# Kernel tuning notes

Measured on AMD Instinct MI355X. Metric: run time of the kernel, lower is better.

Reference implementation:

```python
import jax, jax.numpy as jnp
import numpy as np

B, T, P, C = 32, 16, 16, 2048
EPS = 1e-5


def setup_inputs() -> dict:
    key = jax.random.key(0)
    ks = jax.random.split(key, 9)
    s = 0.02
    return {
        "X": jax.random.normal(ks[0], (B, T, P, C), dtype=jnp.float32),
        "W_att": jax.random.normal(ks[1], (C, C), dtype=jnp.float32) * s,
        "b_att": jnp.zeros((C,), dtype=jnp.float32),
        "W1": jax.random.normal(ks[2], (C, C), dtype=jnp.float32) * s,
        "b1": jnp.zeros((C,), dtype=jnp.float32),
        "gamma": jnp.ones((C,), dtype=jnp.float32),
        "beta": jnp.zeros((C,), dtype=jnp.float32),
        "W2": jax.random.normal(ks[3], (C, C), dtype=jnp.float32) * s,
        "b2": jnp.zeros((C,), dtype=jnp.float32),
    }


def reference(X, W_att, b_att, W1, b1, gamma, beta, W2, b2):
    b, t, p, c = X.shape
    Xf = X.reshape(b * t, p, c)                                   # [BT, P, C]
    # per-frame attention gate: mean over parts -> Linear -> sigmoid
    attn = jax.nn.sigmoid(jnp.einsum("nc,dc->nd", Xf.mean(axis=1), W_att) + b_att)
    Xg = Xf * attn[:, None, :]                                    # gate each part
    # gcn: Linear -> per-frame BatchNorm1d (training stats over P) -> ReLU -> Linear
    h = jnp.einsum("npc,dc->npd", Xg, W1) + b1                    # [BT, P, C]
    mu = h.mean(axis=1, keepdims=True)
    var = jnp.mean(jnp.square(h - mu), axis=1, keepdims=True)     # biased var, as torch BN
    hn = (h - mu) * jax.lax.rsqrt(var + EPS) * gamma + beta
    out = jnp.einsum("npc,dc->npd", jax.nn.relu(hn), W2) + b2
    return out.reshape(b, t, p, c)
```

## Files before the change

kernel.cpp:

```cpp
#include <hip/hip_runtime.h>
#include <hip/hip_bf16.h>

typedef __attribute__((ext_vector_type(8))) short short8;
typedef __attribute__((ext_vector_type(4))) float f32x4;

static constexpr int Cdim = 2048;
static constexpr int NFRM = 512;
static constexpr int Pdim = 16;
static constexpr int MROWS = NFRM * Pdim;
static constexpr float EPS = 1e-5f;

__device__ __forceinline__ unsigned short f2b(float x) {
  union { float f; unsigned u; } v; v.f = x;
  unsigned r = v.u + 0x7fffu + ((v.u >> 16) & 1u);
  return (unsigned short)(r >> 16);
}

__device__ __forceinline__ void gload16(const void* g, void* l) {
  __builtin_amdgcn_global_load_lds(
      (const __attribute__((address_space(1))) unsigned int*)g,
      (__attribute__((address_space(3))) unsigned int*)l, 16, 0, 0);
}


__global__ __launch_bounds__(256) void cast3_kernel(
    const float* __restrict__ s0, const float* __restrict__ s1, const float* __restrict__ s2,
    unsigned short* __restrict__ d0, unsigned short* __restrict__ d1, unsigned short* __restrict__ d2)
{
  long i = (long)blockIdx.x * 256 + threadIdx.x;
  const float* s; unsigned short* d; long off;
  if (i < 1048576)      { s = s0; d = d0; off = i; }
  else if (i < 2097152) { s = s1; d = d1; off = i - 1048576; }
  else                  { s = s2; d = d2; off = i - 2097152; }
  float4 v = reinterpret_cast<const float4*>(s)[off];
  union { unsigned short u[4]; unsigned long long q; } o;
  o.u[0] = f2b(v.x); o.u[1] = f2b(v.y); o.u[2] = f2b(v.z); o.u[3] = f2b(v.w);
  *reinterpret_cast<unsigned long long*>(d + off * 4) = o.q;
}

__global__ __launch_bounds__(256) void mean_cast_kernel(
    const float* __restrict__ X, unsigned short* __restrict__ Mb)
{
  int idx = blockIdx.x * 256 + threadIdx.x;
  int n  = idx >> 9;
  int c4 = idx & 511;
  const float4* xp = reinterpret_cast<const float4*>(X) + (long)n * (Pdim * 512) + c4;
  float4 s = {0.f, 0.f, 0.f, 0.f};
  #pragma unroll
  for (int p = 0; p < Pdim; ++p) {
    float4 v = xp[(long)p * 512];
    s.x += v.x; s.y += v.y; s.z += v.z; s.w += v.w;
  }
  const float r = 1.f / 16.f;
  union { unsigned short u[4]; unsigned long long q; } o;
  o.u[0] = f2b(s.x * r); o.u[1] = f2b(s.y * r); o.u[2] = f2b(s.z * r); o.u[3] = f2b(s.w * r);
  *reinterpret_cast<unsigned long long*>(Mb + (long)idx * 4) = o.q;
}

__global__ __launch_bounds__(256) void gate_kernel(
    const float* __restrict__ X, const float* __restrict__ P0, const float* __restrict__ P1,
    const float* __restrict__ b_att, unsigned short* __restrict__ Xg)
{
  long idx = (long)blockIdx.x * 256 + threadIdx.x;
  int c4 = (int)(idx & 511);
  long np = idx >> 9;
  long n  = np >> 4;
  float4 x  = reinterpret_cast<const float4*>(X)[idx];
  float4 p0 = reinterpret_cast<const float4*>(P0)[n * 512 + c4];
  float4 p1 = reinterpret_cast<const float4*>(P1)[n * 512 + c4];
  float4 bb = reinterpret_cast<const float4*>(b_att)[c4];
  float4 a;
  a.x = 1.f / (1.f + __expf(-(p0.x + p1.x + bb.x)));
  a.y = 1.f / (1.f + __expf(-(p0.y + p1.y + bb.y)));
  a.z = 1.f / (1.f + __expf(-(p0.z + p1.z + bb.z)));
  a.w = 1.f / (1.f + __expf(-(p0.w + p1.w + bb.w)));
  union { unsigned short u[4]; unsigned long long q; } o;
  o.u[0] = f2b(x.x * a.x); o.u[1] = f2b(x.y * a.y);
  o.u[2] = f2b(x.z * a.z); o.u[3] = f2b(x.w * a.w);
  *reinterpret_cast<unsigned long long*>(Xg + idx * 4) = o.q;
}

__global__ __launch_bounds__(256) void gemm_att_sk(
    const unsigned short* __restrict__ A,
    const unsigned short* __restrict__ B,
    float* __restrict__ P)
{
  constexpr int N = 2048, K = 2048, KH = 1024;
  __shared__ unsigned short As[128 * 32];
  __shared__ unsigned short Bs[128 * 32];
  const int t = threadIdx.x;
  const int lane = t & 63;
  const int wid = t >> 6;
  const int wr = wid >> 1, wc = wid & 1;
  const int m0 = blockIdx.x * 128, n0 = blockIdx.y * 128;
  const int k0 = blockIdx.z * KH;
  float* out = P + (long)blockIdx.z * (512L * 2048);

  f32x4 acc[4][4];
  #pragma unroll
  for (int i = 0; i < 4; i++)
    #pragma unroll
    for (int j = 0; j < 4; j++) acc[i][j] = (f32x4){0.f, 0.f, 0.f, 0.f};

  const int srow = t >> 2;
  const int scol = (t & 3) * 8;
  const long aoff0 = (long)(m0 + srow) * K + scol;
  const long aoff1 = (long)(m0 + 64 + srow) * K + scol;
  const long boff0 = (long)(n0 + srow) * K + scol;
  const long boff1 = (long)(n0 + 64 + srow) * K + scol;
  char* AsB = (char*)As;
  char* BsB = (char*)Bs;

  const int fr = lane & 15;
  const int fk = (lane >> 4) * 8;

  for (int kt = k0; kt < k0 + KH; kt += 32) {
    __syncthreads();
    gload16(A + aoff0 + kt, AsB + t * 16);
    gload16(A + aoff1 + kt, AsB + 4096 + t * 16);
    gload16(B + boff0 + kt, BsB + t * 16);
    gload16(B + boff1 + kt, BsB + 4096 + t * 16);
    __syncthreads();
    short8 af[4], bfr[4];
    #pragma unroll
    for (int m = 0; m < 4; m++)
      af[m] = *reinterpret_cast<const short8*>(&As[(wr * 64 + m * 16 + fr) * 32 + fk]);
    #pragma unroll
    for (int n = 0; n < 4; n++)
      bfr[n] = *reinterpret_cast<const short8*>(&Bs[(wc * 64 + n * 16 + fr) * 32 + fk]);
    #pragma unroll
    for (int m = 0; m < 4; m++)
      #pragma unroll
      for (int n = 0; n < 4; n++)
        acc[m][n] = __builtin_amdgcn_mfma_f32_16x16x32_bf16(af[m], bfr[n], acc[m][n], 0, 0, 0);
  }

  const int l4 = lane >> 4;
  #pragma unroll
  for (int m = 0; m < 4; m++) {
    const int r0 = m0 + wr * 64 + m * 16 + l4 * 4;
    #pragma unroll
    for (int n = 0; n < 4; n++) {
      const int cn = n0 + wc * 64 + n * 16 + fr;
      #pragma unroll
      for (int j = 0; j < 4; j++)
        out[(long)(r0 + j) * N + cn] = acc[m][n][j];
    }
  }
}

template<int EPI>
__global__ __launch_bounds__(512, 2) void gemm256(
    const unsigned short* __restrict__ A,
    const unsigned short* __restrict__ Bp,
    int Kk, int Nn, int nbx,
    const float* __restrict__ bias,
    const float* __restrict__ gamma,
    const float* __restrict__ beta,
    float* __restrict__ Cf,
    unsigned short* __restrict__ Cb)
{
  __shared__ char lds[131072];
  const int t = threadIdx.x;
  const int lane = t & 63;
  const int wid = t >> 6;
  const int wr = wid >> 2;
  const int wc = wid & 3;

  const int nw = gridDim.x;
  const int wg = (blockIdx.x & 7) * (nw >> 3) + (blockIdx.x >> 3);
  const int bx = wg % nbx;
  const int by = wg / nbx;
  const int m0 = bx << 8, n0 = by << 8;

  const int NT = Kk >> 6;
  const int NI = NT >> 1;

  const long h64 = (long)64 * Kk, h128 = (long)128 * Kk;
  const int row0 = t >> 3;
  const int col0 = ((t & 7) * 8) ^ ((row0 & 7) << 3);
  const unsigned short* gA = A  + (long)(m0 + row0) * Kk + col0;
  const unsigned short* gB = Bp + (long)(n0 + row0) * Kk + col0;

  const int fr_ = lane & 15;
  const int cb0 = ((lane >> 4) << 4) ^ ((fr_ & 7) << 4);
  const int aB = (wr << 14) + fr_ * 128;
  const int bB = 32768 + ((wc >> 1) << 14) + ((wc & 1) << 13) + fr_ * 128;

#define STG(gp_, ko_, lo_) do { \
    const unsigned short* g0_ = (gp_) + (ko_); \
    gload16(g0_, lds + (lo_) + (t << 4)); \
    gload16(g0_ + h64, lds + (lo_) + 8192 + (t << 4)); } while (0)

#define LDSA(buf_, m_, ks_) (*(const short8*)(lds + (buf_) * 65536 + aB + (m_) * 2048 + (cb0 ^ ((ks_) << 6))))
#define LDSB(buf_, n_, ks_) (*(const short8*)(lds + (buf_) * 65536 + bB + (n_) * 2048 + (cb0 ^ ((ks_) << 6))))

#define RDAF(buf_, mb_) do { \
    af[0][0] = LDSA(buf_, (mb_) + 0, 0); af[0][1] = LDSA(buf_, (mb_) + 0, 1); \
    af[1][0] = LDSA(buf_, (mb_) + 1, 0); af[1][1] = LDSA(buf_, (mb_) + 1, 1); \
    af[2][0] = LDSA(buf_, (mb_) + 2, 0); af[2][1] = LDSA(buf_, (mb_) + 2, 1); \
    af[3][0] = LDSA(buf_, (mb_) + 3, 0); af[3][1] = LDSA(buf_, (mb_) + 3, 1); } while (0)

#define RDB(buf_, nb_, dst_) do { \
    dst_[0][0] = LDSB(buf_, (nb_) + 0, 0); dst_[0][1] = LDSB(buf_, (nb_) + 0, 1); \
    dst_[1][0] = LDSB(buf_, (nb_) + 1, 0); dst_[1][1] = LDSB(buf_, (nb_) + 1, 1); } while (0)

#define QUAD(mb_, nb_, b_) do { \
    _Pragma("unroll") \
    for (int mi = 0; mi < 4; ++mi) { \
      _Pragma("unroll") \
      for (int ni = 0; ni < 2; ++ni) { \
        acc[(mb_) + mi][(nb_) + ni] = __builtin_amdgcn_mfma_f32_16x16x32_bf16(af[mi][0], b_[ni][0], acc[(mb_) + mi][(nb_) + ni], 0, 0, 0); \
        acc[(mb_) + mi][(nb_) + ni] = __builtin_amdgcn_mfma_f32_16x16x32_bf16(af[mi][1], b_[ni][1], acc[(mb_) + mi][(nb_) + ni], 0, 0, 0); \
      } } } while (0)

#define BARX() do { \
    __builtin_amdgcn_sched_barrier(0); \
    __builtin_amdgcn_s_barrier(); \
    asm volatile("s_waitcnt lgkmcnt(0)" ::: "memory"); \
    __builtin_amdgcn_sched_barrier(0); } while (0)

#define PRIO1() __builtin_amdgcn_s_setprio(1)
#define PRIO0() __builtin_amdgcn_s_setprio(0)
#define VMC(n_) asm volatile("s_waitcnt vmcnt(" #n_ ")" ::: "memory")

  f32x4 acc[8][4];
  #pragma unroll
  for (int i = 0; i < 8; i++)
    #pragma unroll
    for (int j = 0; j < 4; j++) acc[i][j] = (f32x4){0.f, 0.f, 0.f, 0.f};

  short8 af[4][2], b23[2][2], b0E[2][2], b0O[2][2];

  STG(gA, 0, 0);
  STG(gA + h128, 0, 16384);
  STG(gB, 0, 32768);
  STG(gB + h128, 0, 49152);
  STG(gB, 64, 98304);
  STG(gB + h128, 64, 114688);
  VMC(4);
  __builtin_amdgcn_s_barrier();
  __builtin_amdgcn_sched_barrier(0);
  RDB(0, 0, b0E);

#define ITERBODY(LAST_) do { \
     \
    STG(gA, ko + 64, 65536); \
    RDAF(0, 0); \
    BARX(); PRIO1(); QUAD(0, 0, b0E); PRIO0(); \
     \
    STG(gA + h128, ko + 64, 81920); \
    RDB(0, 2, b23); \
    BARX(); PRIO1(); QUAD(0, 2, b23); PRIO0(); \
     \
    VMC(4); \
    if (!(LAST_)) STG(gB, ko + 128, 32768); \
    RDAF(0, 4); \
    BARX(); PRIO1(); QUAD(4, 0, b0E); PRIO0(); \
     \
    if (LAST_) { VMC(0); } else { VMC(2); STG(gB + h128, ko + 128, 49152); } \
    RDB(1, 0, b0O); \
    BARX(); PRIO1(); QUAD(4, 2, b23); PRIO0(); \
     \
    if (!(LAST_)) STG(gA, ko + 128, 0); \
    RDAF(1, 0); \
    BARX(); PRIO1(); QUAD(0, 0, b0O); PRIO0(); \
     \
    if (!(LAST_)) STG(gA + h128, ko + 128, 16384); \
    RDB(1, 2, b23); \
    BARX(); PRIO1(); QUAD(0, 2, b23); PRIO0(); \
     \
    if (!(LAST_)) { VMC(4); STG(gB, ko + 192, 98304); } \
    RDAF(1, 4); \
    BARX(); PRIO1(); QUAD(4, 0, b0O); PRIO0(); \
     \
    if (!(LAST_)) { VMC(2); STG(gB + h128, ko + 192, 114688); RDB(0, 0, b0E); } \
    BARX(); PRIO1(); QUAD(4, 2, b23); PRIO0(); \
  } while (0)

  long ko = 0;
  for (int i = 0; i < NI - 1; ++i, ko += 128) {
    ITERBODY(0);
  }
  ITERBODY(1);

  const int l4 = lane >> 4;
  #pragma unroll
  for (int m = 0; m < 8; ++m) {
    const int r0 = m0 + wr * 128 + m * 16 + l4 * 4;
    #pragma unroll
    for (int n = 0; n < 4; ++n) {
      const int cn = n0 + wc * 64 + n * 16 + fr_;
      if constexpr (EPI == 1) {
        float s1 = 0.f, s2 = 0.f;
        #pragma unroll
        for (int j = 0; j < 4; j++) { float v = acc[m][n][j]; s1 += v; s2 += v * v; }
        s1 += __shfl_xor(s1, 16); s2 += __shfl_xor(s2, 16);
        s1 += __shfl_xor(s1, 32); s2 += __shfl_xor(s2, 32);
        const float mean = s1 * 0.0625f;
        const float var  = s2 * 0.0625f - mean * mean;
        const float sc = rsqrtf(var + EPS) * gamma[cn];
        const float sh = beta[cn] - mean * sc;
        #pragma unroll
        for (int j = 0; j < 4; j++) {
          float v = fmaxf(acc[m][n][j] * sc + sh, 0.f);
          Cb[(long)(r0 + j) * Nn + cn] = f2b(v);
        }
      } else {
        const float bb = bias[cn];
        #pragma unroll
        for (int j = 0; j < 4; j++)
          Cf[(long)(r0 + j) * Nn + cn] = acc[m][n][j] + bb;
      }
    }
  }
#undef STG
#undef LDSA
#undef LDSB
#undef RDAF
#undef RDB
#undef QUAD
#undef BARX
#undef PRIO1
#undef PRIO0
#undef VMC
#undef ITERBODY
}

extern "C" void kernel_launch(void* const* d_in, const int* in_sizes, int n_in,
                              void* d_out, int out_size, void* d_ws, size_t ws_size,
                              hipStream_t stream) {
  const float* X     = (const float*)d_in[0];
  const float* W_att = (const float*)d_in[1];
  const float* b_att = (const float*)d_in[2];
  const float* W1    = (const float*)d_in[3];
  const float* gamma = (const float*)d_in[5];
  const float* beta  = (const float*)d_in[6];
  const float* W2    = (const float*)d_in[7];
  const float* b2    = (const float*)d_in[8];
  float* out = (float*)d_out;

  char* ws = (char*)d_ws;
  unsigned short* Wab = (unsigned short*)(ws + 0);
  unsigned short* W1b = (unsigned short*)(ws + 8388608);
  unsigned short* W2b = (unsigned short*)(ws + 16777216);
  float*          Pat = (float*)        (ws + 25165824);
  unsigned short* Xg  = (unsigned short*)(ws + 33554432);
  unsigned short* Hr  = (unsigned short*)(ws + 67108864);
  unsigned short* Mb  = (unsigned short*)(ws + 67108864);

  hipLaunchKernelGGL(cast3_kernel, dim3(12288), dim3(256), 0, stream,
                     W_att, W1, W2, Wab, W1b, W2b);
  hipLaunchKernelGGL(mean_cast_kernel, dim3(1024), dim3(256), 0, stream, X, Mb);
  hipLaunchKernelGGL(gemm_att_sk, dim3(4, 16, 2), dim3(256), 0, stream,
                     Mb, Wab, Pat);
  hipLaunchKernelGGL(gate_kernel, dim3(16384), dim3(256), 0, stream,
                     X, Pat, Pat + 512L * 2048, b_att, Xg);
  hipLaunchKernelGGL((gemm256<1>), dim3(256), dim3(512), 0, stream,
                     Xg, W1b, Cdim, Cdim, 32, nullptr, gamma, beta, nullptr, Hr);
  hipLaunchKernelGGL((gemm256<2>), dim3(256), dim3(512), 0, stream,
                     Hr, W2b, Cdim, Cdim, 32, b2, nullptr, nullptr, out, nullptr);
}
```

Measured before the change: 188.4 us.

## Use 32x32x16 MFMA in main GEMMs and split attention GEMM four ways

The two large 256x256 GEMMs now use the 32x32x16 bf16 MFMA instead of 16x16x32, with new LDS fragment addressing and an epilogue adjusted to the 32x32 accumulator layout, including BatchNorm statistics over 16-row groups. Larger MFMA tiles mean fewer instructions and fewer LDS fragment reads per FLOP. Separately, the attention GEMM split-K goes from 2 to 4 slices to put more blocks on the device, and the gate kernel sums four partials. The extra partial buffer is placed in workspace that aliases the Mb/Hr region, so correctness depends on those buffers not being live at the same time.

```diff
diff --git a/kernel.cpp b/kernel.cpp
--- a/kernel.cpp
+++ b/kernel.cpp
@@ -3,6 +3,7 @@
 
 typedef __attribute__((ext_vector_type(8))) short short8;
 typedef __attribute__((ext_vector_type(4))) float f32x4;
+typedef __attribute__((ext_vector_type(16))) float f32x16;
 
 static constexpr int Cdim = 2048;
 static constexpr int NFRM = 512;
@@ -58,22 +59,25 @@
 }
 
 __global__ __launch_bounds__(256) void gate_kernel(
-    const float* __restrict__ X, const float* __restrict__ P0, const float* __restrict__ P1,
+    const float* __restrict__ X, const float* __restrict__ PA, const float* __restrict__ PB,
     const float* __restrict__ b_att, unsigned short* __restrict__ Xg)
 {
+  constexpr long F = 512L * 2048;
   long idx = (long)blockIdx.x * 256 + threadIdx.x;
   int c4 = (int)(idx & 511);
   long np = idx >> 9;
   long n  = np >> 4;
   float4 x  = reinterpret_cast<const float4*>(X)[idx];
-  float4 p0 = reinterpret_cast<const float4*>(P0)[n * 512 + c4];
-  float4 p1 = reinterpret_cast<const float4*>(P1)[n * 512 + c4];
+  float4 p0 = reinterpret_cast<const float4*>(PA)[n * 512 + c4];
+  float4 p1 = reinterpret_cast<const float4*>(PA + F)[n * 512 + c4];
+  float4 p2 = reinterpret_cast<const float4*>(PB)[n * 512 + c4];
+  float4 p3 = reinterpret_cast<const float4*>(PB + F)[n * 512 + c4];
   float4 bb = reinterpret_cast<const float4*>(b_att)[c4];
   float4 a;
-  a.x = 1.f / (1.f + __expf(-(p0.x + p1.x + bb.x)));
-  a.y = 1.f / (1.f + __expf(-(p0.y + p1.y + bb.y)));
-  a.z = 1.f / (1.f + __expf(-(p0.z + p1.z + bb.z)));
-  a.w = 1.f / (1.f + __expf(-(p0.w + p1.w + bb.w)));
+  a.x = 1.f / (1.f + __expf(-(p0.x + p1.x + p2.x + p3.x + bb.x)));
+  a.y = 1.f / (1.f + __expf(-(p0.y + p1.y + p2.y + p3.y + bb.y)));
+  a.z = 1.f / (1.f + __expf(-(p0.z + p1.z + p2.z + p3.z + bb.z)));
+  a.w = 1.f / (1.f + __expf(-(p0.w + p1.w + p2.w + p3.w + bb.w)));
   union { unsigned short u[4]; unsigned long long q; } o;
   o.u[0] = f2b(x.x * a.x); o.u[1] = f2b(x.y * a.y);
   o.u[2] = f2b(x.z * a.z); o.u[3] = f2b(x.w * a.w);
@@ -83,9 +87,10 @@
 __global__ __launch_bounds__(256) void gemm_att_sk(
     const unsigned short* __restrict__ A,
     const unsigned short* __restrict__ B,
-    float* __restrict__ P)
-{
-  constexpr int N = 2048, K = 2048, KH = 1024;
+    float* __restrict__ PA, float* __restrict__ PB)
+{
+  constexpr int N = 2048, K = 2048, KH = 512;
+  constexpr long F = 512L * 2048;
   __shared__ unsigned short As[128 * 32];
   __shared__ unsigned short Bs[128 * 32];
   const int t = threadIdx.x;
@@ -94,7 +99,7 @@
   const int wr = wid >> 1, wc = wid & 1;
   const int m0 = blockIdx.x * 128, n0 = blockIdx.y * 128;
   const int k0 = blockIdx.z * KH;
-  float* out = P + (long)blockIdx.z * (512L * 2048);
+  float* out = (blockIdx.z < 2) ? (PA + (long)blockIdx.z * F) : (PB + (long)(blockIdx.z - 2) * F);
 
   f32x4 acc[4][4];
   #pragma unroll
@@ -182,36 +187,35 @@
   const unsigned short* gA = A  + (long)(m0 + row0) * Kk + col0;
   const unsigned short* gB = Bp + (long)(n0 + row0) * Kk + col0;
 
-  const int fr_ = lane & 15;
-  const int cb0 = ((lane >> 4) << 4) ^ ((fr_ & 7) << 4);
-  const int aB = (wr << 14) + fr_ * 128;
-  const int bB = 32768 + ((wc >> 1) << 14) + ((wc & 1) << 13) + fr_ * 128;
+  const int fr32 = lane & 31;
+  const int cb32 = (((lane >> 5) << 4)) ^ ((lane & 7) << 4);
+  const int aB32 = (wr << 14) + fr32 * 128;
+  const int bB32 = 32768 + ((wc >> 1) << 14) + (((wc & 1) << 6) + fr32) * 128;
 
 #define STG(gp_, ko_, lo_) do { \
     const unsigned short* g0_ = (gp_) + (ko_); \
     gload16(g0_, lds + (lo_) + (t << 4)); \
     gload16(g0_ + h64, lds + (lo_) + 8192 + (t << 4)); } while (0)
 
-#define LDSA(buf_, m_, ks_) (*(const short8*)(lds + (buf_) * 65536 + aB + (m_) * 2048 + (cb0 ^ ((ks_) << 6))))
-#define LDSB(buf_, n_, ks_) (*(const short8*)(lds + (buf_) * 65536 + bB + (n_) * 2048 + (cb0 ^ ((ks_) << 6))))
-
-#define RDAF(buf_, mb_) do { \
-    af[0][0] = LDSA(buf_, (mb_) + 0, 0); af[0][1] = LDSA(buf_, (mb_) + 0, 1); \
-    af[1][0] = LDSA(buf_, (mb_) + 1, 0); af[1][1] = LDSA(buf_, (mb_) + 1, 1); \
-    af[2][0] = LDSA(buf_, (mb_) + 2, 0); af[2][1] = LDSA(buf_, (mb_) + 2, 1); \
-    af[3][0] = LDSA(buf_, (mb_) + 3, 0); af[3][1] = LDSA(buf_, (mb_) + 3, 1); } while (0)
-
-#define RDB(buf_, nb_, dst_) do { \
-    dst_[0][0] = LDSB(buf_, (nb_) + 0, 0); dst_[0][1] = LDSB(buf_, (nb_) + 0, 1); \
-    dst_[1][0] = LDSB(buf_, (nb_) + 1, 0); dst_[1][1] = LDSB(buf_, (nb_) + 1, 1); } while (0)
-
-#define QUAD(mb_, nb_, b_) do { \
+#define LDSA32(buf_, mh_, ml_, ks_) (*(const short8*)(lds + (buf_) * 65536 + aB32 + (mh_) * 8192 + (ml_) * 4096 + (cb32 ^ ((ks_) << 5))))
+#define LDSB32(buf_, nh_, ks_)      (*(const short8*)(lds + (buf_) * 65536 + bB32 + (nh_) * 4096 + (cb32 ^ ((ks_) << 5))))
+
+#define RDA32(buf_, mh_) do { \
+    af[0][0] = LDSA32(buf_, mh_, 0, 0); af[0][1] = LDSA32(buf_, mh_, 0, 1); \
+    af[0][2] = LDSA32(buf_, mh_, 0, 2); af[0][3] = LDSA32(buf_, mh_, 0, 3); \
+    af[1][0] = LDSA32(buf_, mh_, 1, 0); af[1][1] = LDSA32(buf_, mh_, 1, 1); \
+    af[1][2] = LDSA32(buf_, mh_, 1, 2); af[1][3] = LDSA32(buf_, mh_, 1, 3); } while (0)
+
+#define RDB32(buf_, nh_, dst_) do { \
+    dst_[0] = LDSB32(buf_, nh_, 0); dst_[1] = LDSB32(buf_, nh_, 1); \
+    dst_[2] = LDSB32(buf_, nh_, 2); dst_[3] = LDSB32(buf_, nh_, 3); } while (0)
+
+#define QUAD32(mh_, nh_, b_) do { \
     _Pragma("unroll") \
-    for (int mi = 0; mi < 4; ++mi) { \
+    for (int ml = 0; ml < 2; ++ml) { \
       _Pragma("unroll") \
-      for (int ni = 0; ni < 2; ++ni) { \
-        acc[(mb_) + mi][(nb_) + ni] = __builtin_amdgcn_mfma_f32_16x16x32_bf16(af[mi][0], b_[ni][0], acc[(mb_) + mi][(nb_) + ni], 0, 0, 0); \
-        acc[(mb_) + mi][(nb_) + ni] = __builtin_amdgcn_mfma_f32_16x16x32_bf16(af[mi][1], b_[ni][1], acc[(mb_) + mi][(nb_) + ni], 0, 0, 0); \
+      for (int ks = 0; ks < 4; ++ks) { \
+        acc[(mh_) * 2 + ml][nh_] = __builtin_amdgcn_mfma_f32_32x32x16_bf16(af[ml][ks], b_[ks], acc[(mh_) * 2 + ml][nh_], 0, 0, 0); \
       } } } while (0)
 
 #define BARX() do { \
@@ -224,13 +228,15 @@
 #define PRIO0() __builtin_amdgcn_s_setprio(0)
 #define VMC(n_) asm volatile("s_waitcnt vmcnt(" #n_ ")" ::: "memory")
 
-  f32x4 acc[8][4];
-  #pragma unroll
-  for (int i = 0; i < 8; i++)
-    #pragma unroll
-    for (int j = 0; j < 4; j++) acc[i][j] = (f32x4){0.f, 0.f, 0.f, 0.f};
-
-  short8 af[4][2], b23[2][2], b0E[2][2], b0O[2][2];
+  f32x16 acc[4][2];
+  #pragma unroll
+  for (int i = 0; i < 4; i++)
+    #pragma unroll
+    for (int j = 0; j < 2; j++)
+      #pragma unroll
+      for (int e = 0; e < 16; e++) acc[i][j][e] = 0.f;
+
+  short8 af[2][4], b1s[4], bE0[4], bO0[4];
 
   STG(gA, 0, 0);
   STG(gA + h128, 0, 16384);
@@ -241,41 +247,41 @@
   VMC(4);
   __builtin_amdgcn_s_barrier();
   __builtin_amdgcn_sched_barrier(0);
-  RDB(0, 0, b0E);
+  RDB32(0, 0, bE0);
 
 #define ITERBODY(LAST_) do { \
      \
     STG(gA, ko + 64, 65536); \
-    RDAF(0, 0); \
-    BARX(); PRIO1(); QUAD(0, 0, b0E); PRIO0(); \
+    RDA32(0, 0); \
+    BARX(); PRIO1(); QUAD32(0, 0, bE0); PRIO0(); \
      \
     STG(gA + h128, ko + 64, 81920); \
-    RDB(0, 2, b23); \
-    BARX(); PRIO1(); QUAD(0, 2, b23); PRIO0(); \
+    RDB32(0, 1, b1s); \
+    BARX(); PRIO1(); QUAD32(0, 1, b1s); PRIO0(); \
      \
     VMC(4); \
     if (!(LAST_)) STG(gB, ko + 128, 32768); \
-    RDAF(0, 4); \
-    BARX(); PRIO1(); QUAD(4, 0, b0E); PRIO0(); \
+    RDA32(0, 1); \
+    BARX(); PRIO1(); QUAD32(1, 0, bE0); PRIO0(); \
      \
     if (LAST_) { VMC(0); } else { VMC(2); STG(gB + h128, ko + 128, 49152); } \
-    RDB(1, 0, b0O); \
-    BARX(); PRIO1(); QUAD(4, 2, b23); PRIO0(); \
+    RDB32(1, 0, bO0); \
+    BARX(); PRIO1(); QUAD32(1, 1, b1s); PRIO0(); \
      \
     if (!(LAST_)) STG(gA, ko + 128, 0); \
-    RDAF(1, 0); \
-    BARX(); PRIO1(); QUAD(0, 0, b0O); PRIO0(); \
+    RDA32(1, 0); \
+    BARX(); PRIO1(); QUAD32(0, 0, bO0); PRIO0(); \
      \
     if (!(LAST_)) STG(gA + h128, ko + 128, 16384); \
-    RDB(1, 2, b23); \
-    BARX(); PRIO1(); QUAD(0, 2, b23); PRIO0(); \
+    RDB32(1, 1, b1s); \
+    BARX(); PRIO1(); QUAD32(0, 1, b1s); PRIO0(); \
      \
     if (!(LAST_)) { VMC(4); STG(gB, ko + 192, 98304); } \
-    RDAF(1, 4); \
-    BARX(); PRIO1(); QUAD(4, 0, b0O); PRIO0(); \
-     \
-    if (!(LAST_)) { VMC(2); STG(gB + h128, ko + 192, 114688); RDB(0, 0, b0E); } \
-    BARX(); PRIO1(); QUAD(4, 2, b23); PRIO0(); \
+    RDA32(1, 1); \
+    BARX(); PRIO1(); QUAD32(1, 0, bO0); PRIO0(); \
+     \
+    if (!(LAST_)) { VMC(2); STG(gB + h128, ko + 192, 114688); RDB32(0, 0, bE0); } \
+    BARX(); PRIO1(); QUAD32(1, 1, b1s); PRIO0(); \
   } while (0)
 
   long ko = 0;
@@ -284,42 +290,48 @@
   }
   ITERBODY(1);
 
-  const int l4 = lane >> 4;
-  #pragma unroll
-  for (int m = 0; m < 8; ++m) {
-    const int r0 = m0 + wr * 128 + m * 16 + l4 * 4;
-    #pragma unroll
-    for (int n = 0; n < 4; ++n) {
-      const int cn = n0 + wc * 64 + n * 16 + fr_;
+  const int hi = lane >> 5;
+  #pragma unroll
+  for (int mt = 0; mt < 4; ++mt) {
+    const int rbase = m0 + wr * 128 + mt * 32;
+    #pragma unroll
+    for (int nh = 0; nh < 2; ++nh) {
+      const int cn = n0 + wc * 64 + nh * 32 + fr32;
       if constexpr (EPI == 1) {
-        float s1 = 0.f, s2 = 0.f;
+        const float g_ = gamma[cn], b_ = beta[cn];
         #pragma unroll
-        for (int j = 0; j < 4; j++) { float v = acc[m][n][j]; s1 += v; s2 += v * v; }
-        s1 += __shfl_xor(s1, 16); s2 += __shfl_xor(s2, 16);
-        s1 += __shfl_xor(s1, 32); s2 += __shfl_xor(s2, 32);
-        const float mean = s1 * 0.0625f;
-        const float var  = s2 * 0.0625f - mean * mean;
-        const float sc = rsqrtf(var + EPS) * gamma[cn];
-        const float sh = beta[cn] - mean * sc;
-        #pragma unroll
-        for (int j = 0; j < 4; j++) {
-          float v = fmaxf(acc[m][n][j] * sc + sh, 0.f);
-          Cb[(long)(r0 + j) * Nn + cn] = f2b(v);
+        for (int f = 0; f < 2; ++f) {
+          float s1 = 0.f, s2 = 0.f;
+          #pragma unroll
+          for (int j = 0; j < 8; ++j) { float v = acc[mt][nh][f * 8 + j]; s1 += v; s2 += v * v; }
+          s1 += __shfl_xor(s1, 32); s2 += __shfl_xor(s2, 32);
+          const float mean = s1 * 0.0625f;
+          const float var  = s2 * 0.0625f - mean * mean;
+          const float sc = rsqrtf(var + EPS) * g_;
+          const float sh = b_ - mean * sc;
+          #pragma unroll
+          for (int j = 0; j < 8; ++j) {
+            const int row = rbase + f * 16 + (j & 3) + 8 * (j >> 2) + 4 * hi;
+            float v = fmaxf(acc[mt][nh][f * 8 + j] * sc + sh, 0.f);
+            Cb[(long)row * Nn + cn] = f2b(v);
+          }
         }
       } else {
         const float bb = bias[cn];
         #pragma unroll
-        for (int j = 0; j < 4; j++)
-          Cf[(long)(r0 + j) * Nn + cn] = acc[m][n][j] + bb;
+        for (int r = 0; r < 16; ++r) {
+          const int row = rbase + (r & 3) + 8 * (r >> 2) + 4 * hi;
+          Cf[(long)row * Nn + cn] = acc[mt][nh][r] + bb;
+        }
       }
     }
   }
 #undef STG
-#undef LDSA
-#undef LDSB
-#undef RDAF
-#undef RDB
-#undef QUAD
+#undef LDSA32
+#undef LDSB32
+#undef RDA32
+#undef RDB32
+#undef QUAD32
 #undef BARX
 #undef PRIO1
 #undef PRIO0
@@ -344,18 +356,19 @@
   unsigned short* Wab = (unsigned short*)(ws + 0);
   unsigned short* W1b = (unsigned short*)(ws + 8388608);
   unsigned short* W2b = (unsigned short*)(ws + 16777216);
-  float*          Pat = (float*)        (ws + 25165824);
+  float*          PatA= (float*)        (ws + 25165824);
   unsigned short* Xg  = (unsigned short*)(ws + 33554432);
   unsigned short* Hr  = (unsigned short*)(ws + 67108864);
   unsigned short* Mb  = (unsigned short*)(ws + 67108864);
+  float*          PatB= (float*)        (ws + 67108864 + 2097152);
 
   hipLaunchKernelGGL(cast3_kernel, dim3(12288), dim3(256), 0, stream,
                      W_att, W1, W2, Wab, W1b, W2b);
   hipLaunchKernelGGL(mean_cast_kernel, dim3(1024), dim3(256), 0, stream, X, Mb);
-  hipLaunchKernelGGL(gemm_att_sk, dim3(4, 16, 2), dim3(256), 0, stream,
-                     Mb, Wab, Pat);
+  hipLaunchKernelGGL(gemm_att_sk, dim3(4, 16, 4), dim3(256), 0, stream,
+                     Mb, Wab, PatA, PatB);
   hipLaunchKernelGGL(gate_kernel, dim3(16384), dim3(256), 0, stream,
-                     X, Pat, Pat + 512L * 2048, b_att, Xg);
+                     X, PatA, PatB, b_att, Xg);
   hipLaunchKernelGGL((gemm256<1>), dim3(256), dim3(512), 0, stream,
                      Xg, W1b, Cdim, Cdim, 32, nullptr, gamma, beta, nullptr, Hr);
   hipLaunchKernelGGL((gemm256<2>), dim3(256), dim3(512), 0, stream,
```

Result: slower. 201.9 us (+7.1%).

## Raise attention GEMM split-K to four and double-buffer A fragments in main GEMM

Applied to the files above, without the earlier changes.

The attention-gate GEMM now splits K four ways instead of two, giving 256 blocks instead of 128 so more CUs have work; the gate kernel sums four partial buffers, with the extra two stored in a second workspace region. The main 256-tile GEMM pipeline is reworked so A fragments use two register sets and the next LDS reads are issued right after each barrier. Partial lgkmcnt waits replace the full wait, so LDS reads overlap the MFMA work. This costs more registers and extra partial-sum traffic, and depends on the waitcnt counts being exactly right.

```diff
diff --git a/kernel.cpp b/kernel.cpp
--- a/kernel.cpp
+++ b/kernel.cpp
@@ -58,22 +58,25 @@
 }
 
 __global__ __launch_bounds__(256) void gate_kernel(
-    const float* __restrict__ X, const float* __restrict__ P0, const float* __restrict__ P1,
+    const float* __restrict__ X, const float* __restrict__ PA, const float* __restrict__ PB,
     const float* __restrict__ b_att, unsigned short* __restrict__ Xg)
 {
+  constexpr long F = 512L * 2048;
   long idx = (long)blockIdx.x * 256 + threadIdx.x;
   int c4 = (int)(idx & 511);
   long np = idx >> 9;
   long n  = np >> 4;
   float4 x  = reinterpret_cast<const float4*>(X)[idx];
-  float4 p0 = reinterpret_cast<const float4*>(P0)[n * 512 + c4];
-  float4 p1 = reinterpret_cast<const float4*>(P1)[n * 512 + c4];
+  float4 p0 = reinterpret_cast<const float4*>(PA)[n * 512 + c4];
+  float4 p1 = reinterpret_cast<const float4*>(PA + F)[n * 512 + c4];
+  float4 p2 = reinterpret_cast<const float4*>(PB)[n * 512 + c4];
+  float4 p3 = reinterpret_cast<const float4*>(PB + F)[n * 512 + c4];
   float4 bb = reinterpret_cast<const float4*>(b_att)[c4];
   float4 a;
-  a.x = 1.f / (1.f + __expf(-(p0.x + p1.x + bb.x)));
-  a.y = 1.f / (1.f + __expf(-(p0.y + p1.y + bb.y)));
-  a.z = 1.f / (1.f + __expf(-(p0.z + p1.z + bb.z)));
-  a.w = 1.f / (1.f + __expf(-(p0.w + p1.w + bb.w)));
+  a.x = 1.f / (1.f + __expf(-(p0.x + p1.x + p2.x + p3.x + bb.x)));
+  a.y = 1.f / (1.f + __expf(-(p0.y + p1.y + p2.y + p3.y + bb.y)));
+  a.z = 1.f / (1.f + __expf(-(p0.z + p1.z + p2.z + p3.z + bb.z)));
+  a.w = 1.f / (1.f + __expf(-(p0.w + p1.w + p2.w + p3.w + bb.w)));
   union { unsigned short u[4]; unsigned long long q; } o;
   o.u[0] = f2b(x.x * a.x); o.u[1] = f2b(x.y * a.y);
   o.u[2] = f2b(x.z * a.z); o.u[3] = f2b(x.w * a.w);
@@ -83,9 +86,10 @@
 __global__ __launch_bounds__(256) void gemm_att_sk(
     const unsigned short* __restrict__ A,
     const unsigned short* __restrict__ B,
-    float* __restrict__ P)
-{
-  constexpr int N = 2048, K = 2048, KH = 1024;
+    float* __restrict__ PA, float* __restrict__ PB)
+{
+  constexpr int N = 2048, K = 2048, KH = 512;
+  constexpr long F = 512L * 2048;
   __shared__ unsigned short As[128 * 32];
   __shared__ unsigned short Bs[128 * 32];
   const int t = threadIdx.x;
@@ -94,7 +98,7 @@
   const int wr = wid >> 1, wc = wid & 1;
   const int m0 = blockIdx.x * 128, n0 = blockIdx.y * 128;
   const int k0 = blockIdx.z * KH;
-  float* out = P + (long)blockIdx.z * (512L * 2048);
+  float* out = (blockIdx.z < 2) ? (PA + (long)blockIdx.z * F) : (PB + (long)(blockIdx.z - 2) * F);
 
   f32x4 acc[4][4];
   #pragma unroll
@@ -195,29 +199,32 @@
 #define LDSA(buf_, m_, ks_) (*(const short8*)(lds + (buf_) * 65536 + aB + (m_) * 2048 + (cb0 ^ ((ks_) << 6))))
 #define LDSB(buf_, n_, ks_) (*(const short8*)(lds + (buf_) * 65536 + bB + (n_) * 2048 + (cb0 ^ ((ks_) << 6))))
 
-#define RDAF(buf_, mb_) do { \
-    af[0][0] = LDSA(buf_, (mb_) + 0, 0); af[0][1] = LDSA(buf_, (mb_) + 0, 1); \
-    af[1][0] = LDSA(buf_, (mb_) + 1, 0); af[1][1] = LDSA(buf_, (mb_) + 1, 1); \
-    af[2][0] = LDSA(buf_, (mb_) + 2, 0); af[2][1] = LDSA(buf_, (mb_) + 2, 1); \
-    af[3][0] = LDSA(buf_, (mb_) + 3, 0); af[3][1] = LDSA(buf_, (mb_) + 3, 1); } while (0)
+#define RDAF(buf_, mb_, dst_) do { \
+    dst_[0][0] = LDSA(buf_, (mb_) + 0, 0); dst_[0][1] = LDSA(buf_, (mb_) + 0, 1); \
+    dst_[1][0] = LDSA(buf_, (mb_) + 1, 0); dst_[1][1] = LDSA(buf_, (mb_) + 1, 1); \
+    dst_[2][0] = LDSA(buf_, (mb_) + 2, 0); dst_[2][1] = LDSA(buf_, (mb_) + 2, 1); \
+    dst_[3][0] = LDSA(buf_, (mb_) + 3, 0); dst_[3][1] = LDSA(buf_, (mb_) + 3, 1); } while (0)
 
 #define RDB(buf_, nb_, dst_) do { \
     dst_[0][0] = LDSB(buf_, (nb_) + 0, 0); dst_[0][1] = LDSB(buf_, (nb_) + 0, 1); \
     dst_[1][0] = LDSB(buf_, (nb_) + 1, 0); dst_[1][1] = LDSB(buf_, (nb_) + 1, 1); } while (0)
 
-#define QUAD(mb_, nb_, b_) do { \
+#define QUAD(mb_, nb_, a_, b_) do { \
     _Pragma("unroll") \
     for (int mi = 0; mi < 4; ++mi) { \
       _Pragma("unroll") \
       for (int ni = 0; ni < 2; ++ni) { \
-        acc[(mb_) + mi][(nb_) + ni] = __builtin_amdgcn_mfma_f32_16x16x32_bf16(af[mi][0], b_[ni][0], acc[(mb_) + mi][(nb_) + ni], 0, 0, 0); \
-        acc[(mb_) + mi][(nb_) + ni] = __builtin_amdgcn_mfma_f32_16x16x32_bf16(af[mi][1], b_[ni][1], acc[(mb_) + mi][(nb_) + ni], 0, 0, 0); \
+        acc[(mb_) + mi][(nb_) + ni] = __builtin_amdgcn_mfma_f32_16x16x32_bf16(a_[mi][0], b_[ni][0], acc[(mb_) + mi][(nb_) + ni], 0, 0, 0); \
+        acc[(mb_) + mi][(nb_) + ni] = __builtin_amdgcn_mfma_f32_16x16x32_bf16(a_[mi][1], b_[ni][1], acc[(mb_) + mi][(nb_) + ni], 0, 0, 0); \
       } } } while (0)
 
 #define BARX() do { \
     __builtin_amdgcn_sched_barrier(0); \
     __builtin_amdgcn_s_barrier(); \
-    asm volatile("s_waitcnt lgkmcnt(0)" ::: "memory"); \
+    __builtin_amdgcn_sched_barrier(0); } while (0)
+
+#define LGK(n_) do { \
+    asm volatile("s_waitcnt lgkmcnt(" #n_ ")" ::: "memory"); \
     __builtin_amdgcn_sched_barrier(0); } while (0)
 
 #define PRIO1() __builtin_amdgcn_s_setprio(1)
@@ -230,7 +237,7 @@
     #pragma unroll
     for (int j = 0; j < 4; j++) acc[i][j] = (f32x4){0.f, 0.f, 0.f, 0.f};
 
-  short8 af[4][2], b23[2][2], b0E[2][2], b0O[2][2];
+  short8 afA[4][2], afB[4][2], b23[2][2], bE0[2][2], bO0[2][2];
 
   STG(gA, 0, 0);
   STG(gA + h128, 0, 16384);
@@ -241,41 +248,51 @@
   VMC(4);
   __builtin_amdgcn_s_barrier();
   __builtin_amdgcn_sched_barrier(0);
-  RDB(0, 0, b0E);
+  RDAF(0, 0, afA);
+  RDB(0, 0, bE0);
+  __builtin_amdgcn_sched_barrier(0);
 
 #define ITERBODY(LAST_) do { \
      \
     STG(gA, ko + 64, 65536); \
-    RDAF(0, 0); \
-    BARX(); PRIO1(); QUAD(0, 0, b0E); PRIO0(); \
+    BARX(); \
+    RDB(0, 2, b23); \
+    LGK(4); PRIO1(); QUAD(0, 0, afA, bE0); PRIO0(); \
      \
     STG(gA + h128, ko + 64, 81920); \
-    RDB(0, 2, b23); \
-    BARX(); PRIO1(); QUAD(0, 2, b23); PRIO0(); \
-     \
-    VMC(4); \
-    if (!(LAST_)) STG(gB, ko + 128, 32768); \
-    RDAF(0, 4); \
-    BARX(); PRIO1(); QUAD(4, 0, b0E); PRIO0(); \
-     \
-    if (LAST_) { VMC(0); } else { VMC(2); STG(gB + h128, ko + 128, 49152); } \
-    RDB(1, 0, b0O); \
-    BARX(); PRIO1(); QUAD(4, 2, b23); PRIO0(); \
+    BARX(); \
+    RDAF(0, 4, afB); \
+    LGK(8); PRIO1(); QUAD(0, 2, afA, b23); PRIO0(); \
+     \
+    if (LAST_) { VMC(6); } else { VMC(8); STG(gB, ko + 128, 32768); } \
+    BARX(); \
+    RDB(1, 0, bO0); \
+    LGK(4); PRIO1(); QUAD(4, 0, afB, bE0); PRIO0(); \
+     \
+    if (LAST_) { VMC(0); } else { VMC(4); STG(gB + h128, ko + 128, 49152); } \
+    BARX(); \
+    RDAF(1, 0, afA); \
+    LGK(12); PRIO1(); QUAD(4, 2, afB, b23); PRIO0(); \
      \
     if (!(LAST_)) STG(gA, ko + 128, 0); \
-    RDAF(1, 0); \
-    BARX(); PRIO1(); QUAD(0, 0, b0O); PRIO0(); \
+    BARX(); \
+    RDB(1, 2, b23); \
+    LGK(4); PRIO1(); QUAD(0, 0, afA, bO0); PRIO0(); \
      \
     if (!(LAST_)) STG(gA + h128, ko + 128, 16384); \
-    RDB(1, 2, b23); \
-    BARX(); PRIO1(); QUAD(0, 2, b23); PRIO0(); \
-     \
-    if (!(LAST_)) { VMC(4); STG(gB, ko + 192, 98304); } \
-    RDAF(1, 4); \
-    BARX(); PRIO1(); QUAD(4, 0, b0O); PRIO0(); \
-     \
-    if (!(LAST_)) { VMC(2); STG(gB + h128, ko + 192, 114688); RDB(0, 0, b0E); } \
-    BARX(); PRIO1(); QUAD(4, 2, b23); PRIO0(); \
+    BARX(); \
+    RDAF(1, 4, afB); \
+    LGK(8); PRIO1(); QUAD(0, 2, afA, b23); PRIO0(); \
+     \
+    if (!(LAST_)) { VMC(8); STG(gB, ko + 192, 98304); } \
+    BARX(); \
+    if (!(LAST_)) { RDB(0, 0, bE0); LGK(4); } else { LGK(0); } \
+    PRIO1(); QUAD(4, 0, afB, bO0); PRIO0(); \
+     \
+    if (!(LAST_)) { VMC(4); STG(gB + h128, ko + 192, 114688); } \
+    BARX(); \
+    if (!(LAST_)) { RDAF(0, 0, afA); LGK(12); } else { LGK(0); } \
+    PRIO1(); QUAD(4, 2, afB, b23); PRIO0(); \
   } while (0)
 
   long ko = 0;
@@ -321,6 +338,7 @@
 #undef RDB
 #undef QUAD
 #undef BARX
+#undef LGK
 #undef PRIO1
 #undef PRIO0
 #undef VMC
@@ -344,18 +362,19 @@
   unsigned short* Wab = (unsigned short*)(ws + 0);
   unsigned short* W1b = (unsigned short*)(ws + 8388608);
   unsigned short* W2b = (unsigned short*)(ws + 16777216);
-  float*          Pat = (float*)        (ws + 25165824);
+  float*          PatA= (float*)        (ws + 25165824);
   unsigned short* Xg  = (unsigned short*)(ws + 33554432);
   unsigned short* Hr  = (unsigned short*)(ws + 67108864);
   unsigned short* Mb  = (unsigned short*)(ws + 67108864);
+  float*          PatB= (float*)        (ws + 67108864 + 2097152);
 
   hipLaunchKernelGGL(cast3_kernel, dim3(12288), dim3(256), 0, stream,
                      W_att, W1, W2, Wab, W1b, W2b);
   hipLaunchKernelGGL(mean_cast_kernel, dim3(1024), dim3(256), 0, stream, X, Mb);
-  hipLaunchKernelGGL(gemm_att_sk, dim3(4, 16, 2), dim3(256), 0, stream,
-                     Mb, Wab, Pat);
+  hipLaunchKernelGGL(gemm_att_sk, dim3(4, 16, 4), dim3(256), 0, stream,
+                     Mb, Wab, PatA, PatB);
   hipLaunchKernelGGL(gate_kernel, dim3(16384), dim3(256), 0, stream,
-                     X, Pat, Pat + 512L * 2048, b_att, Xg);
+                     X, PatA, PatB, b_att, Xg);
   hipLaunchKernelGGL((gemm256<1>), dim3(256), dim3(512), 0, stream,
                      Xg, W1b, Cdim, Cdim, 32, nullptr, gamma, beta, nullptr, Hr);
   hipLaunchKernelGGL((gemm256<2>), dim3(256), dim3(512), 0, stream,
```

Measured after the change: 469.6 us. 149% more time.

## Split attention GEMM four ways along K and drop LDS wait in barrier macro

Applied to the files above, without the earlier changes.

The attention-gate GEMM now splits K into four slices instead of two, launching twice as many blocks. This gives the 512x2048 problem more parallelism across the CUs. The gate kernel now sums four partial buffers, and the extra two partials live in a workspace region that is later reused for Hr. Separately, the explicit lgkmcnt(0) wait is removed from the barrier macro in the main GEMM pipeline to cut stalls. That relies on the compiler's own waits for LDS reads and risks races with the async global-to-LDS stores.

```diff
diff --git a/kernel.cpp b/kernel.cpp
--- a/kernel.cpp
+++ b/kernel.cpp
@@ -58,22 +58,25 @@
 }
 
 __global__ __launch_bounds__(256) void gate_kernel(
-    const float* __restrict__ X, const float* __restrict__ P0, const float* __restrict__ P1,
+    const float* __restrict__ X, const float* __restrict__ PA, const float* __restrict__ PB,
     const float* __restrict__ b_att, unsigned short* __restrict__ Xg)
 {
+  constexpr long F = 512L * 2048;
   long idx = (long)blockIdx.x * 256 + threadIdx.x;
   int c4 = (int)(idx & 511);
   long np = idx >> 9;
   long n  = np >> 4;
   float4 x  = reinterpret_cast<const float4*>(X)[idx];
-  float4 p0 = reinterpret_cast<const float4*>(P0)[n * 512 + c4];
-  float4 p1 = reinterpret_cast<const float4*>(P1)[n * 512 + c4];
+  float4 p0 = reinterpret_cast<const float4*>(PA)[n * 512 + c4];
+  float4 p1 = reinterpret_cast<const float4*>(PA + F)[n * 512 + c4];
+  float4 p2 = reinterpret_cast<const float4*>(PB)[n * 512 + c4];
+  float4 p3 = reinterpret_cast<const float4*>(PB + F)[n * 512 + c4];
   float4 bb = reinterpret_cast<const float4*>(b_att)[c4];
   float4 a;
-  a.x = 1.f / (1.f + __expf(-(p0.x + p1.x + bb.x)));
-  a.y = 1.f / (1.f + __expf(-(p0.y + p1.y + bb.y)));
-  a.z = 1.f / (1.f + __expf(-(p0.z + p1.z + bb.z)));
-  a.w = 1.f / (1.f + __expf(-(p0.w + p1.w + bb.w)));
+  a.x = 1.f / (1.f + __expf(-(p0.x + p1.x + p2.x + p3.x + bb.x)));
+  a.y = 1.f / (1.f + __expf(-(p0.y + p1.y + p2.y + p3.y + bb.y)));
+  a.z = 1.f / (1.f + __expf(-(p0.z + p1.z + p2.z + p3.z + bb.z)));
+  a.w = 1.f / (1.f + __expf(-(p0.w + p1.w + p2.w + p3.w + bb.w)));
   union { unsigned short u[4]; unsigned long long q; } o;
   o.u[0] = f2b(x.x * a.x); o.u[1] = f2b(x.y * a.y);
   o.u[2] = f2b(x.z * a.z); o.u[3] = f2b(x.w * a.w);
@@ -83,9 +86,10 @@
 __global__ __launch_bounds__(256) void gemm_att_sk(
     const unsigned short* __restrict__ A,
     const unsigned short* __restrict__ B,
-    float* __restrict__ P)
-{
-  constexpr int N = 2048, K = 2048, KH = 1024;
+    float* __restrict__ PA, float* __restrict__ PB)
+{
+  constexpr int N = 2048, K = 2048, KH = 512;
+  constexpr long F = 512L * 2048;
   __shared__ unsigned short As[128 * 32];
   __shared__ unsigned short Bs[128 * 32];
   const int t = threadIdx.x;
@@ -94,7 +98,7 @@
   const int wr = wid >> 1, wc = wid & 1;
   const int m0 = blockIdx.x * 128, n0 = blockIdx.y * 128;
   const int k0 = blockIdx.z * KH;
-  float* out = P + (long)blockIdx.z * (512L * 2048);
+  float* out = (blockIdx.z < 2) ? (PA + (long)blockIdx.z * F) : (PB + (long)(blockIdx.z - 2) * F);
 
   f32x4 acc[4][4];
   #pragma unroll
@@ -217,7 +221,6 @@
 #define BARX() do { \
     __builtin_amdgcn_sched_barrier(0); \
     __builtin_amdgcn_s_barrier(); \
-    asm volatile("s_waitcnt lgkmcnt(0)" ::: "memory"); \
     __builtin_amdgcn_sched_barrier(0); } while (0)
 
 #define PRIO1() __builtin_amdgcn_s_setprio(1)
@@ -230,7 +233,7 @@
     #pragma unroll
     for (int j = 0; j < 4; j++) acc[i][j] = (f32x4){0.f, 0.f, 0.f, 0.f};
 
-  short8 af[4][2], b23[2][2], b0E[2][2], b0O[2][2];
+  short8 af[4][2], b23[2][2], bE0[2][2], bO0[2][2];
 
   STG(gA, 0, 0);
   STG(gA + h128, 0, 16384);
@@ -241,13 +244,13 @@
   VMC(4);
   __builtin_amdgcn_s_barrier();
   __builtin_amdgcn_sched_barrier(0);
-  RDB(0, 0, b0E);
+  RDB(0, 0, bE0);
 
 #define ITERBODY(LAST_) do { \
      \
     STG(gA, ko + 64, 65536); \
     RDAF(0, 0); \
-    BARX(); PRIO1(); QUAD(0, 0, b0E); PRIO0(); \
+    BARX(); PRIO1(); QUAD(0, 0, bE0); PRIO0(); \
      \
     STG(gA + h128, ko + 64, 81920); \
     RDB(0, 2, b23); \
@@ -256,15 +259,15 @@
     VMC(4); \
     if (!(LAST_)) STG(gB, ko + 128, 32768); \
     RDAF(0, 4); \
-    BARX(); PRIO1(); QUAD(4, 0, b0E); PRIO0(); \
+    BARX(); PRIO1(); QUAD(4, 0, bE0); PRIO0(); \
      \
     if (LAST_) { VMC(0); } else { VMC(2); STG(gB + h128, ko + 128, 49152); } \
-    RDB(1, 0, b0O); \
+    RDB(1, 0, bO0); \
     BARX(); PRIO1(); QUAD(4, 2, b23); PRIO0(); \
      \
     if (!(LAST_)) STG(gA, ko + 128, 0); \
     RDAF(1, 0); \
-    BARX(); PRIO1(); QUAD(0, 0, b0O); PRIO0(); \
+    BARX(); PRIO1(); QUAD(0, 0, bO0); PRIO0(); \
      \
     if (!(LAST_)) STG(gA + h128, ko + 128, 16384); \
     RDB(1, 2, b23); \
@@ -272,9 +275,9 @@
      \
     if (!(LAST_)) { VMC(4); STG(gB, ko + 192, 98304); } \
     RDAF(1, 4); \
-    BARX(); PRIO1(); QUAD(4, 0, b0O); PRIO0(); \
-     \
-    if (!(LAST_)) { VMC(2); STG(gB + h128, ko + 192, 114688); RDB(0, 0, b0E); } \
+    BARX(); PRIO1(); QUAD(4, 0, bO0); PRIO0(); \
+     \
+    if (!(LAST_)) { VMC(2); STG(gB + h128, ko + 192, 114688); RDB(0, 0, bE0); } \
     BARX(); PRIO1(); QUAD(4, 2, b23); PRIO0(); \
   } while (0)
 
@@ -344,18 +347,19 @@
   unsigned short* Wab = (unsigned short*)(ws + 0);
   unsigned short* W1b = (unsigned short*)(ws + 8388608);
   unsigned short* W2b = (unsigned short*)(ws + 16777216);
-  float*          Pat = (float*)        (ws + 25165824);
+  float*          PatA= (float*)        (ws + 25165824);
   unsigned short* Xg  = (unsigned short*)(ws + 33554432);
   unsigned short* Hr  = (unsigned short*)(ws + 67108864);
   unsigned short* Mb  = (unsigned short*)(ws + 67108864);
+  float*          PatB= (float*)        (ws + 67108864 + 2097152);
 
   hipLaunchKernelGGL(cast3_kernel, dim3(12288), dim3(256), 0, stream,
                      W_att, W1, W2, Wab, W1b, W2b);
   hipLaunchKernelGGL(mean_cast_kernel, dim3(1024), dim3(256), 0, stream, X, Mb);
-  hipLaunchKernelGGL(gemm_att_sk, dim3(4, 16, 2), dim3(256), 0, stream,
-                     Mb, Wab, Pat);
+  hipLaunchKernelGGL(gemm_att_sk, dim3(4, 16, 4), dim3(256), 0, stream,
+                     Mb, Wab, PatA, PatB);
   hipLaunchKernelGGL(gate_kernel, dim3(16384), dim3(256), 0, stream,
-                     X, Pat, Pat + 512L * 2048, b_att, Xg);
+                     X, PatA, PatB, b_att, Xg);
   hipLaunchKernelGGL((gemm256<1>), dim3(256), dim3(512), 0, stream,
                      Xg, W1b, Cdim, Cdim, 32, nullptr, gamma, beta, nullptr, Hr);
   hipLaunchKernelGGL((gemm256<2>), dim3(256), dim3(512), 0, stream,
```

Measured after the change: 183.9 us. 2.4% less time.
